# Kernel tuning notes

Measured on AMD Instinct MI355X. Metric: run time of the kernel, lower is better.

The kernel has to match this reference:

```python
import jax, jax.numpy as jnp
import numpy as np

B, L = 16, 1024
D_MODEL = 384
EXPAND = 2
D_INNER = EXPAND * D_MODEL  # 768
D_STATE = 16
D_CONV = 4
DT_RANK = (D_MODEL + 15) // 16  # 24


def _causal_conv(x, w, b):
    # x: (B,L,Di); w: (Di,K) depthwise kernel; b: (Di,). Causal: pad K-1 on the left.
    K = w.shape[1]
    Lx = x.shape[1]
    xp = jnp.pad(x, ((0, 0), (K - 1, 0), (0, 0)))
    out = sum(xp[:, k:k + Lx, :] * w[:, k] for k in range(K)) + b
    return out


def _selective_scan(u, delta, A, Bm, Cm, Dv):
    # u, delta: (B,L,Di); A: (Di,N); Bm, Cm: (B,L,N); Dv: (Di,)
    def step(h, inp):
        dt, bt, ct, ut = inp  # (B,Di),(B,N),(B,N),(B,Di)
        dA = jnp.exp(dt[..., None] * A)                     # (B,Di,N)
        h = h * dA + (dt * ut)[..., None] * bt[:, None, :]  # (B,Di,N)
        y = jnp.einsum('bdn,bn->bd', h, ct)
        return h, y

    h0 = jnp.zeros((u.shape[0], u.shape[2], A.shape[1]), u.dtype)
    xs = (delta.swapaxes(0, 1), Bm.swapaxes(0, 1), Cm.swapaxes(0, 1), u.swapaxes(0, 1))
    _, ys = jax.lax.scan(step, h0, xs)
    return ys.swapaxes(0, 1) + u * Dv


def _mamba_dir(xz, conv_w, conv_bias, xproj_w, dt_w, dt_b, A_log, Dv):
    xh, z = jnp.split(xz, 2, axis=-1)                 # each (B,L,Di)
    xh = jax.nn.silu(_causal_conv(xh, conv_w, conv_bias))
    dbc = xh @ xproj_w.T                              # (B,L,DT_RANK+2N)
    dt, Bm, Cm = jnp.split(dbc, [DT_RANK, DT_RANK + D_STATE], axis=-1)
    delta = jax.nn.softplus(dt @ dt_w.T + dt_b)       # (B,L,Di)
    A = -jnp.exp(A_log)                               # (Di,N)
    y = _selective_scan(xh, delta, A, Bm, Cm, Dv)
    return y * jax.nn.silu(z)


def setup_inputs():
    key = jax.random.key(0)
    ks = jax.random.split(key, 16)

    def rn(k, shape, s):
        return jax.random.normal(k, shape, dtype=jnp.float32) * s

    A_init = jnp.log(jnp.tile(jnp.arange(1, D_STATE + 1, dtype=jnp.float32), (D_INNER, 1)))
    return dict(
        x=rn(ks[0], (B, L, D_MODEL), 1.0),
        ln_w=jnp.ones((D_MODEL,), jnp.float32),
        ln_b=jnp.zeros((D_MODEL,), jnp.float32),
        in_proj_w=rn(ks[1], (2 * D_INNER, D_MODEL), 0.02),
        out_proj_w=rn(ks[2], (D_MODEL, D_INNER), 0.02),
        conv_w_fwd=rn(ks[3], (D_INNER, D_CONV), 0.2),
        conv_bias_fwd=jnp.zeros((D_INNER,), jnp.float32),
        xproj_w_fwd=rn(ks[4], (DT_RANK + 2 * D_STATE, D_INNER), 0.02),
        dt_w_fwd=rn(ks[5], (D_INNER, DT_RANK), 0.1),
        dt_b_fwd=jnp.full((D_INNER,), -4.0, jnp.float32),
        A_log_fwd=A_init,
        D_fwd=jnp.ones((D_INNER,), jnp.float32),
        conv_w_bwd=rn(ks[6], (D_INNER, D_CONV), 0.2),
        conv_bias_bwd=jnp.zeros((D_INNER,), jnp.float32),
        xproj_w_bwd=rn(ks[7], (DT_RANK + 2 * D_STATE, D_INNER), 0.02),
        dt_w_bwd=rn(ks[8], (D_INNER, DT_RANK), 0.1),
        dt_b_bwd=jnp.full((D_INNER,), -4.0, jnp.float32),
        A_log_bwd=A_init,
        D_bwd=jnp.ones((D_INNER,), jnp.float32),
    )


def reference(x, ln_w, ln_b, in_proj_w, out_proj_w,
              conv_w_fwd, conv_bias_fwd, xproj_w_fwd, dt_w_fwd, dt_b_fwd, A_log_fwd, D_fwd,
              conv_w_bwd, conv_bias_bwd, xproj_w_bwd, dt_w_bwd, dt_b_bwd, A_log_bwd, D_bwd):
    # LayerNorm
    mu = x.mean(-1, keepdims=True)
    var = ((x - mu) ** 2).mean(-1, keepdims=True)
    xn = (x - mu) / jnp.sqrt(var + 1e-5) * ln_w + ln_b
    # Shared input projection -> (B,L,2*Di)
    xz = xn @ in_proj_w.T
    # Forward-direction mamba branch
    out_f = _mamba_dir(xz, conv_w_fwd, conv_bias_fwd, xproj_w_fwd, dt_w_fwd, dt_b_fwd, A_log_fwd, D_fwd)
    # Backward-direction branch on sequence-flipped xz, flipped back (bimamba v2)
    out_r = _mamba_dir(xz[:, ::-1], conv_w_bwd, conv_bias_bwd, xproj_w_bwd, dt_w_bwd, dt_b_bwd, A_log_bwd, D_bwd)[:, ::-1]
    # Output projection + residual (drop_path=0 -> identity)
    return x + (out_f + out_r) @ out_proj_w.T
```

## Files before the change

kernel.cpp:

```cpp
#include <hip/hip_runtime.h>
#include <cstdint>
#include <cstddef>

#define BN_   16
#define LN_   1024
#define DM_   384
#define DI_   768
#define NS_   16
#define RDT_  24
#define NDBC_ 56
#define NDBCP 64
#define NC_   16
#define LC_   64

typedef unsigned short ushortT;
typedef short bf16x8 __attribute__((ext_vector_type(8)));
typedef float f32x4 __attribute__((ext_vector_type(4)));

typedef __attribute__((address_space(3))) uint32_t lds_u32_t;
typedef __attribute__((address_space(1))) const uint32_t glb_u32_t;

static __device__ __forceinline__ void stage16(const void* g, void* lds) {
    __builtin_amdgcn_global_load_lds(
        (glb_u32_t*)(uintptr_t)g,
        (lds_u32_t*)(uint32_t)(uintptr_t)lds,
        16, 0, 0);
}

static __device__ __forceinline__ float silu_f(float x) {
    return x / (1.0f + __expf(-x));
}
static __device__ __forceinline__ float softplus_f(float s) {
    return fmaxf(s, 0.0f) + __logf(1.0f + __expf(-fabsf(s)));
}
static __device__ __forceinline__ ushortT f2bf(float f) {
    union { float f; uint32_t u; } v; v.f = f;
    uint32_t u = v.u;
    uint32_t r = u + 0x7fffu + ((u >> 16) & 1u);
    return (ushortT)(r >> 16);
}
static __device__ __forceinline__ float bf2f(ushortT b) {
    union { uint32_t u; float f; } v; v.u = ((uint32_t)b) << 16;
    return v.f;
}

__global__ __launch_bounds__(256) void wconv_kernel(
    const float* __restrict__ w1, int n1, const float* __restrict__ w2, int n2,
    const float* __restrict__ xwf, const float* __restrict__ xwb,
    ushortT* __restrict__ o1, ushortT* __restrict__ o2,
    ushortT* __restrict__ oxf, ushortT* __restrict__ oxb)
{
    int i = blockIdx.x * 256 + threadIdx.x;
    if (i < n1) { o1[i] = f2bf(w1[i]); return; }
    i -= n1;
    if (i < n2) { o2[i] = f2bf(w2[i]); return; }
    i -= n2;
    const int nx = NDBCP * DI_;
    if (i < 2 * nx) {
        int which = i >= nx;
        int j = which ? (i - nx) : i;
        int row = j / DI_;
        const float* src = which ? xwb : xwf;
        ushortT* dst = which ? oxb : oxf;
        dst[j] = (row < NDBC_) ? f2bf(src[j]) : (ushortT)0;
    }
}

__global__ __launch_bounds__(256) void ln_kernel(
    const float* __restrict__ x, const float* __restrict__ w,
    const float* __restrict__ b, ushortT* __restrict__ xn,
    int row0, int nrows)
{
    int r = blockIdx.x * 4 + (threadIdx.x >> 6);
    if (r >= nrows) return;
    int lane = threadIdx.x & 63;
    const float* xr = x + (size_t)(row0 + r) * DM_;
    float v[6];
    float s = 0.0f;
#pragma unroll
    for (int i = 0; i < 6; i++) { v[i] = xr[lane + 64 * i]; s += v[i]; }
#pragma unroll
    for (int o = 32; o > 0; o >>= 1) s += __shfl_down(s, o, 64);
    s = __shfl(s, 0, 64);
    float mu = s * (1.0f / DM_);
    float q = 0.0f;
#pragma unroll
    for (int i = 0; i < 6; i++) { float d = v[i] - mu; q += d * d; }
#pragma unroll
    for (int o = 32; o > 0; o >>= 1) q += __shfl_down(q, o, 64);
    q = __shfl(q, 0, 64);
    float rstd = rsqrtf(q * (1.0f / DM_) + 1e-5f);
    ushortT* outp = xn + (size_t)r * DM_;
#pragma unroll
    for (int i = 0; i < 6; i++) {
        int c = lane + 64 * i;
        outp[c] = f2bf((v[i] - mu) * rstd * w[c] + b[c]);
    }
}

template <int BM, int BN, int WR, int WC, bool CAT, bool RES, bool OB>
__global__ __launch_bounds__(256) void gemm_mfma(
    const ushortT* __restrict__ Aa, const ushortT* __restrict__ Ab_,
    const ushortT* __restrict__ W, const float* __restrict__ R,
    void* __restrict__ Cv, int M, int N, int Khalf)
{
    constexpr int WTM = BM / WR;
    constexpr int WTN = BN / WC;
    constexpr int FM = WTM / 16;
    constexpr int FN = WTN / 16;
    __shared__ ushortT As[BM * 32];
    __shared__ ushortT Ws[BN * 32];
    int tid = threadIdx.x;
    int bm = blockIdx.x * BM, bn = blockIdx.y * BN;
    int wave = tid >> 6, lane = tid & 63;
    int wm = wave % WR, wn = wave / WR;
    f32x4 acc[FM][FN] = {};
    int Ktot = CAT ? 2 * Khalf : Khalf;
    int lrow = lane >> 2;
    int lk = (lane & 3) * 8;

    for (int k0 = 0; k0 < Ktot; k0 += 32) {
        const ushortT* Asrc = (!CAT || k0 < Khalf) ? Aa : Ab_;
        int ka = (!CAT || k0 < Khalf) ? k0 : (k0 - Khalf);
        __syncthreads();
#pragma unroll
        for (int c = 0; c < BM / 64; c++) {
            int ch = c * 4 + wave;
            int row = ch * 16 + lrow;
            stage16(Asrc + (size_t)(bm + row) * Khalf + ka + lk, &As[ch * 16 * 32]);
        }
#pragma unroll
        for (int c = 0; c < BN / 64; c++) {
            int ch = c * 4 + wave;
            int row = ch * 16 + lrow;
            stage16(W + (size_t)(bn + row) * Khalf + ka + lk, &Ws[ch * 16 * 32]);
        }
        __syncthreads();
        int mb = (wm * WTM + (lane & 15)) * 32 + (lane >> 4) * 8;
        int nb = (wn * WTN + (lane & 15)) * 32 + (lane >> 4) * 8;
        bf16x8 af[FM], bfr[FN];
#pragma unroll
        for (int mi = 0; mi < FM; mi++) af[mi] = *(bf16x8*)&As[mb + mi * 16 * 32];
#pragma unroll
        for (int ni = 0; ni < FN; ni++) bfr[ni] = *(bf16x8*)&Ws[nb + ni * 16 * 32];
#pragma unroll
        for (int mi = 0; mi < FM; mi++)
#pragma unroll
            for (int ni = 0; ni < FN; ni++)
                acc[mi][ni] = __builtin_amdgcn_mfma_f32_16x16x32_bf16(
                    af[mi], bfr[ni], acc[mi][ni], 0, 0, 0);
    }

#pragma unroll
    for (int mi = 0; mi < FM; mi++) {
        int row = bm + wm * WTM + 16 * mi + (lane >> 4) * 4;
#pragma unroll
        for (int ni = 0; ni < FN; ni++) {
            int col = bn + wn * WTN + 16 * ni + (lane & 15);
#pragma unroll
            for (int r = 0; r < 4; r++) {
                size_t o = (size_t)(row + r) * N + col;
                float v = acc[mi][ni][r];
                if (RES) v += R[o];
                if (OB) ((ushortT*)Cv)[o] = f2bf(v);
                else    ((float*)Cv)[o] = v;
            }
        }
    }
}

__global__ __launch_bounds__(256) void conv_kernel(
    const ushortT* __restrict__ XZ,
    const float* __restrict__ wf, const float* __restrict__ bf,
    const float* __restrict__ wb, const float* __restrict__ bb,
    ushortT* __restrict__ XH, int gB)
{
    const int D8 = DI_ / 8;
    int idx = blockIdx.x * 256 + threadIdx.x;
    int perdir = gB * LN_ * D8;
    int dir = 0;
    if (idx >= perdir) { idx -= perdir; dir = 1; }
    int d8 = idx % D8;
    int l = (idx / D8) & (LN_ - 1);
    int b = idx / (D8 * LN_);
    int d = d8 * 8;
    const float* cw = (dir ? wb : wf) + d * 4;
    const float* cb = (dir ? bb : bf) + d;

    float xv[4][8];
#pragma unroll
    for (int k = 0; k < 4; k++) {
        int j = l - 3 + k;
        if (j < 0) {
#pragma unroll
            for (int c = 0; c < 8; c++) xv[k][c] = 0.0f;
        } else {
            int ls = dir ? (LN_ - 1 - j) : j;
            ushort4 v = *(const ushort4*)(XZ + (size_t)(b * LN_ + ls) * (2 * DI_) + d);
            ushort4 v2 = *(const ushort4*)(XZ + (size_t)(b * LN_ + ls) * (2 * DI_) + d + 4);
            xv[k][0] = bf2f(v.x);  xv[k][1] = bf2f(v.y);
            xv[k][2] = bf2f(v.z);  xv[k][3] = bf2f(v.w);
            xv[k][4] = bf2f(v2.x); xv[k][5] = bf2f(v2.y);
            xv[k][6] = bf2f(v2.z); xv[k][7] = bf2f(v2.w);
        }
    }
    ushortT out[8];
#pragma unroll
    for (int c = 0; c < 8; c++) {
        float4 w4 = *(const float4*)(cw + c * 4);
        float s = cb[c];
        s = fmaf(xv[0][c], w4.x, s);
        s = fmaf(xv[1][c], w4.y, s);
        s = fmaf(xv[2][c], w4.z, s);
        s = fmaf(xv[3][c], w4.w, s);
        out[c] = f2bf(silu_f(s));
    }
    ushortT* op = XH + ((size_t)dir * gB * LN_ + (size_t)(b * LN_ + l)) * DI_ + d;
    *(ushort4*)(op + 0) = make_ushort4(out[0], out[1], out[2], out[3]);
    *(ushort4*)(op + 4) = make_ushort4(out[4], out[5], out[6], out[7]);
}

__global__ __launch_bounds__(256) void xproj_mfma(
    const ushortT* __restrict__ XH, const ushortT* __restrict__ Wf,
    const ushortT* __restrict__ Wb, float* __restrict__ Cf,
    float* __restrict__ Cb, int mblocksPerDir)
{
    __shared__ ushortT As[64 * 32];
    __shared__ ushortT Ws[64 * 32];
    int blk = blockIdx.x;
    int dir = blk >= mblocksPerDir;
    const ushortT* W = dir ? Wb : Wf;
    float* C = dir ? Cb : Cf;
    int bmG = blk * 64;
    int bmC = (blk - dir * mblocksPerDir) * 64;
    int tid = threadIdx.x, wave = tid >> 6, lane = tid & 63;
    f32x4 acc[4] = {};
    int lrow = lane >> 2;
    int lk = (lane & 3) * 8;

    for (int k0 = 0; k0 < DI_; k0 += 32) {
        __syncthreads();
        stage16(XH + (size_t)(bmG + wave * 16 + lrow) * DI_ + k0 + lk, &As[wave * 16 * 32]);
        stage16(W + (size_t)(wave * 16 + lrow) * DI_ + k0 + lk, &Ws[wave * 16 * 32]);
        __syncthreads();
        bf16x8 bfr = *(bf16x8*)&Ws[(wave * 16 + (lane & 15)) * 32 + (lane >> 4) * 8];
#pragma unroll
        for (int mi = 0; mi < 4; mi++) {
            bf16x8 af = *(bf16x8*)&As[(mi * 16 + (lane & 15)) * 32 + (lane >> 4) * 8];
            acc[mi] = __builtin_amdgcn_mfma_f32_16x16x32_bf16(af, bfr, acc[mi], 0, 0, 0);
        }
    }
#pragma unroll
    for (int mi = 0; mi < 4; mi++) {
        int row = bmC + 16 * mi + (lane >> 4) * 4;
        int col = wave * 16 + (lane & 15);
#pragma unroll
        for (int r = 0; r < 4; r++)
            C[(size_t)(row + r) * NDBCP + col] = acc[mi][r];
    }
}

__global__ __launch_bounds__(256) void scan1_kernel(
    const ushortT* __restrict__ XH,
    const float* __restrict__ dbcf, const float* __restrict__ dbcb,
    const float* __restrict__ dtwf, const float* __restrict__ dtbf,
    const float* __restrict__ alogf,
    const float* __restrict__ dtwb, const float* __restrict__ dtbb,
    const float* __restrict__ alogb,
    uint32_t* __restrict__ UD,
    float* __restrict__ hs1, float* __restrict__ dec, int gB)
{
    int bid = blockIdx.x;
    int c = bid % NC_; bid /= NC_;
    int dchunk = bid % 3; bid /= 3;
    int b = bid % gB;
    int dir = bid / gB;
    int d = dchunk * 256 + threadIdx.x;

    const ushortT* xh = XH + (size_t)dir * gB * LN_ * DI_;
    const float* dbc  = dir ? dbcb : dbcf;
    const float* dtw  = (dir ? dtwb : dtwf) + d * RDT_;
    float dtb         = (dir ? dtbb : dtbf)[d];
    const float* alog = dir ? alogb : alogf;

    float An[NS_];
#pragma unroll
    for (int n = 0; n < NS_; n++) An[n] = -__expf(alog[d * NS_ + n]);
    float a1 = An[0];
    bool pk = true;
#pragma unroll
    for (int n = 0; n < NS_; n++)
        pk = pk && (fabsf(An[n] - (float)(n + 1) * a1) <=
                    1e-3f * (float)(n + 1) * fabsf(a1) + 1e-6f);
    pk = (bool)__all((int)pk);

    float wrow[RDT_];
#pragma unroll
    for (int r = 0; r < RDT_; r++) wrow[r] = dtw[r];

    __shared__ float sdbc[LC_ * NDBCP];
    int rb = b * LN_ + c * LC_;
    int jb = c * LC_;
#pragma unroll
    for (int i = 0; i < 4; i++) {
        int idx = threadIdx.x + 256 * i;
        int row = idx >> 4, c4 = (idx & 15) * 4;
        *(float4*)&sdbc[row * NDBCP + c4] =
            *(const float4*)(dbc + (size_t)(rb + row) * NDBCP + c4);
    }
    __syncthreads();

    float h[NS_];
#pragma unroll
    for (int n = 0; n < NS_; n++) h[n] = 0.0f;
    float S = 0.0f;
    uint32_t* udp = UD + (size_t)((dir * gB + b) * LN_ + jb) * DI_ + d;

    if (pk) {
        for (int lr = 0; lr < LC_; lr++) {
            const float4* rp4 = (const float4*)&sdbc[lr * NDBCP];
            float4 t0 = rp4[0], t1 = rp4[1], t2 = rp4[2];
            float4 t3 = rp4[3], t4 = rp4[4], t5 = rp4[5];
            float s0 = dtb, s1 = 0.f, s2 = 0.f, s3 = 0.f;
            s0 = fmaf(t0.x, wrow[0], s0);  s1 = fmaf(t0.y, wrow[1], s1);
            s2 = fmaf(t0.z, wrow[2], s2);  s3 = fmaf(t0.w, wrow[3], s3);
            s0 = fmaf(t1.x, wrow[4], s0);  s1 = fmaf(t1.y, wrow[5], s1);
            s2 = fmaf(t1.z, wrow[6], s2);  s3 = fmaf(t1.w, wrow[7], s3);
            s0 = fmaf(t2.x, wrow[8], s0);  s1 = fmaf(t2.y, wrow[9], s1);
            s2 = fmaf(t2.z, wrow[10], s2); s3 = fmaf(t2.w, wrow[11], s3);
            s0 = fmaf(t3.x, wrow[12], s0); s1 = fmaf(t3.y, wrow[13], s1);
            s2 = fmaf(t3.z, wrow[14], s2); s3 = fmaf(t3.w, wrow[15], s3);
            s0 = fmaf(t4.x, wrow[16], s0); s1 = fmaf(t4.y, wrow[17], s1);
            s2 = fmaf(t4.z, wrow[18], s2); s3 = fmaf(t4.w, wrow[19], s3);
            s0 = fmaf(t5.x, wrow[20], s0); s1 = fmaf(t5.y, wrow[21], s1);
            s2 = fmaf(t5.z, wrow[22], s2); s3 = fmaf(t5.w, wrow[23], s3);
            float dt = softplus_f((s0 + s1) + (s2 + s3));
            S += dt;
            float u = bf2f(xh[(rb + lr) * DI_ + d]);
            udp[lr * DI_] = ((uint32_t)f2bf(dt) << 16) | (uint32_t)f2bf(u);
            float du = dt * u;
            float4 B0 = rp4[6], B1 = rp4[7], B2 = rp4[8], B3 = rp4[9];
            const float* Bp = (const float*)&B0;
            float Bv[NS_] = {B0.x, B0.y, B0.z, B0.w, B1.x, B1.y, B1.z, B1.w,
                             B2.x, B2.y, B2.z, B2.w, B3.x, B3.y, B3.z, B3.w};
            (void)Bp;
            float q1 = __expf(dt * a1);
            float q2 = q1 * q1, q4 = q2 * q2, q8 = q4 * q4;
            float p2 = q2, p3 = q2 * q1, p5 = q4 * q1, p6 = q4 * q2, p7 = q4 * p3;
            float pw[NS_] = {q1, p2, p3, q4, p5, p6, p7, q8,
                             q8 * q1, q8 * p2, q8 * p3, q8 * q4,
                             q8 * p5, q8 * p6, q8 * p7, q8 * q8};
#pragma unroll
            for (int n = 0; n < NS_; n++)
                h[n] = fmaf(h[n], pw[n], du * Bv[n]);
        }
        float q1 = __expf(S * a1);
        float q2 = q1 * q1, q4 = q2 * q2, q8 = q4 * q4;
        float p2 = q2, p3 = q2 * q1, p5 = q4 * q1, p6 = q4 * q2, p7 = q4 * p3;
        float pw[NS_] = {q1, p2, p3, q4, p5, p6, p7, q8,
                         q8 * q1, q8 * p2, q8 * p3, q8 * q4,
                         q8 * p5, q8 * p6, q8 * p7, q8 * q8};
        int si = (((dir * gB + b) * NC_ + c) * DI_ + d) * NS_;
#pragma unroll
        for (int n = 0; n < NS_; n++) {
            hs1[si + n] = h[n];
            dec[si + n] = pw[n];
        }
    } else {
        for (int lr = 0; lr < LC_; lr++) {
            const float* rowp = &sdbc[lr * NDBCP];
            float s0 = dtb, s1 = 0.f, s2 = 0.f, s3 = 0.f;
#pragma unroll
            for (int r = 0; r < 6; r++) {
                s0 = fmaf(rowp[r], wrow[r], s0);
                s1 = fmaf(rowp[6 + r], wrow[6 + r], s1);
                s2 = fmaf(rowp[12 + r], wrow[12 + r], s2);
                s3 = fmaf(rowp[18 + r], wrow[18 + r], s3);
            }
            float dt = softplus_f((s0 + s1) + (s2 + s3));
            S += dt;
            float u = bf2f(xh[(rb + lr) * DI_ + d]);
            udp[lr * DI_] = ((uint32_t)f2bf(dt) << 16) | (uint32_t)f2bf(u);
            float du = dt * u;
#pragma unroll
            for (int n = 0; n < NS_; n++)
                h[n] = fmaf(h[n], __expf(dt * An[n]), du * rowp[RDT_ + n]);
        }
        int si = (((dir * gB + b) * NC_ + c) * DI_ + d) * NS_;
#pragma unroll
        for (int n = 0; n < NS_; n++) {
            hs1[si + n] = h[n];
            dec[si + n] = __expf(An[n] * S);
        }
    }
}

__global__ __launch_bounds__(256) void scan2_kernel(
    const float* __restrict__ hs1, const float* __restrict__ dec,
    float* __restrict__ hin, int gB)
{
    int e = blockIdx.x * 256 + threadIdx.x;
    int n = e & 15; int e2 = e >> 4;
    int d = e2 % DI_; e2 /= DI_;
    int b = e2 % gB; int dir = e2 / gB;
    int base = (((dir * gB + b) * NC_) * DI_ + d) * NS_ + n;
    float h = 0.0f;
    const int cs = DI_ * NS_;
    for (int c = 0; c < NC_; c++) {
        int idx = base + c * cs;
        hin[idx] = h;
        h = fmaf(h, dec[idx], hs1[idx]);
    }
}

__global__ __launch_bounds__(256) void scan3_kernel(
    const uint32_t* __restrict__ UD, const ushortT* __restrict__ XZ,
    const float* __restrict__ dbcf, const float* __restrict__ dbcb,
    const float* __restrict__ alogf, const float* __restrict__ dvf,
    const float* __restrict__ alogb, const float* __restrict__ dvb,
    const float* __restrict__ hin,
    ushortT* __restrict__ yf, ushortT* __restrict__ yb, int gB)
{
    int bid = blockIdx.x;
    int c = bid % NC_; bid /= NC_;
    int dchunk = bid % 3; bid /= 3;
    int b = bid % gB;
    int dir = bid / gB;
    int d = dchunk * 256 + threadIdx.x;

    const float* dbc  = dir ? dbcb : dbcf;
    const float* alog = dir ? alogb : alogf;
    float Dd          = (dir ? dvb : dvf)[d];
    ushortT* y        = dir ? yb : yf;

    float An[NS_];
#pragma unroll
    for (int n = 0; n < NS_; n++) An[n] = -__expf(alog[d * NS_ + n]);
    float a1 = An[0];
    bool pk = true;
#pragma unroll
    for (int n = 0; n < NS_; n++)
        pk = pk && (fabsf(An[n] - (float)(n + 1) * a1) <=
                    1e-3f * (float)(n + 1) * fabsf(a1) + 1e-6f);
    pk = (bool)__all((int)pk);

    __shared__ float sBC[LC_ * 32];
    int rb = b * LN_ + c * LC_;
    int jb = c * LC_;
#pragma unroll
    for (int i = 0; i < 2; i++) {
        int idx = threadIdx.x + 256 * i;
        int row = idx >> 3, c4 = (idx & 7) * 4;
        *(float4*)&sBC[row * 32 + c4] =
            *(const float4*)(dbc + (size_t)(rb + row) * NDBCP + RDT_ + c4);
    }
    __syncthreads();

    int si = (((dir * gB + b) * NC_ + c) * DI_ + d) * NS_;
    float h[NS_];
#pragma unroll
    for (int n = 0; n < NS_; n++) h[n] = hin[si + n];
    const uint32_t* udp = UD + (size_t)((dir * gB + b) * LN_ + jb) * DI_ + d;

    if (pk) {
        for (int lr = 0; lr < LC_; lr++) {
            const float4* rp4 = (const float4*)&sBC[lr * 32];
            float4 B0 = rp4[0], B1 = rp4[1], B2 = rp4[2], B3 = rp4[3];
            float4 C0 = rp4[4], C1 = rp4[5], C2 = rp4[6], C3 = rp4[7];
            float Bv[NS_] = {B0.x, B0.y, B0.z, B0.w, B1.x, B1.y, B1.z, B1.w,
                             B2.x, B2.y, B2.z, B2.w, B3.x, B3.y, B3.z, B3.w};
            float Cw[NS_] = {C0.x, C0.y, C0.z, C0.w, C1.x, C1.y, C1.z, C1.w,
                             C2.x, C2.y, C2.z, C2.w, C3.x, C3.y, C3.z, C3.w};
            uint32_t ud = udp[lr * DI_];
            float u = bf2f((ushortT)(ud & 0xffffu));
            float dt = bf2f((ushortT)(ud >> 16));
            float du = dt * u;
            float q1 = __expf(dt * a1);
            float q2 = q1 * q1, q4 = q2 * q2, q8 = q4 * q4;
            float p2 = q2, p3 = q2 * q1, p5 = q4 * q1, p6 = q4 * q2, p7 = q4 * p3;
            float pw[NS_] = {q1, p2, p3, q4, p5, p6, p7, q8,
                             q8 * q1, q8 * p2, q8 * p3, q8 * q4,
                             q8 * p5, q8 * p6, q8 * p7, q8 * q8};
            float y0 = 0.f, y1 = 0.f, y2 = 0.f, y3 = 0.f;
#pragma unroll
            for (int n = 0; n < NS_; n += 4) {
                h[n + 0] = fmaf(h[n + 0], pw[n + 0], du * Bv[n + 0]);
                h[n + 1] = fmaf(h[n + 1], pw[n + 1], du * Bv[n + 1]);
                h[n + 2] = fmaf(h[n + 2], pw[n + 2], du * Bv[n + 2]);
                h[n + 3] = fmaf(h[n + 3], pw[n + 3], du * Bv[n + 3]);
                y0 = fmaf(h[n + 0], Cw[n + 0], y0);
                y1 = fmaf(h[n + 1], Cw[n + 1], y1);
                y2 = fmaf(h[n + 2], Cw[n + 2], y2);
                y3 = fmaf(h[n + 3], Cw[n + 3], y3);
            }
            float yv = ((y0 + y1) + (y2 + y3)) + u * Dd;
            int j = jb + lr;
            int lo = dir ? (LN_ - 1 - j) : j;
            float z = bf2f(XZ[(size_t)(b * LN_ + lo) * (2 * DI_) + DI_ + d]);
            y[(b * LN_ + lo) * DI_ + d] = f2bf(yv * silu_f(z));
        }
    } else {
        for (int lr = 0; lr < LC_; lr++) {
            const float* rowp = &sBC[lr * 32];
            uint32_t ud = udp[lr * DI_];
            float u = bf2f((ushortT)(ud & 0xffffu));
            float dt = bf2f((ushortT)(ud >> 16));
            float du = dt * u;
            float y0 = 0.f, y1 = 0.f, y2 = 0.f, y3 = 0.f;
#pragma unroll
            for (int n = 0; n < NS_; n += 4) {
                h[n + 0] = fmaf(h[n + 0], __expf(dt * An[n + 0]), du * rowp[n + 0]);
                h[n + 1] = fmaf(h[n + 1], __expf(dt * An[n + 1]), du * rowp[n + 1]);
                h[n + 2] = fmaf(h[n + 2], __expf(dt * An[n + 2]), du * rowp[n + 2]);
                h[n + 3] = fmaf(h[n + 3], __expf(dt * An[n + 3]), du * rowp[n + 3]);
                y0 = fmaf(h[n + 0], rowp[16 + n + 0], y0);
                y1 = fmaf(h[n + 1], rowp[16 + n + 1], y1);
                y2 = fmaf(h[n + 2], rowp[16 + n + 2], y2);
                y3 = fmaf(h[n + 3], rowp[16 + n + 3], y3);
            }
            float yv = ((y0 + y1) + (y2 + y3)) + u * Dd;
            int j = jb + lr;
            int lo = dir ? (LN_ - 1 - j) : j;
            float z = bf2f(XZ[(size_t)(b * LN_ + lo) * (2 * DI_) + DI_ + d]);
            y[(b * LN_ + lo) * DI_ + d] = f2bf(yv * silu_f(z));
        }
    }
}

extern "C" void kernel_launch(void* const* d_in, const int* in_sizes, int n_in,
                              void* d_out, int out_size, void* d_ws, size_t ws_size,
                              hipStream_t stream)
{
    const float* x         = (const float*)d_in[0];
    const float* ln_w      = (const float*)d_in[1];
    const float* ln_b      = (const float*)d_in[2];
    const float* in_proj_w = (const float*)d_in[3];
    const float* out_proj_w= (const float*)d_in[4];
    const float* conv_wf   = (const float*)d_in[5];
    const float* conv_bf   = (const float*)d_in[6];
    const float* xproj_f   = (const float*)d_in[7];
    const float* dt_wf     = (const float*)d_in[8];
    const float* dt_bf     = (const float*)d_in[9];
    const float* alog_f    = (const float*)d_in[10];
    const float* dv_f      = (const float*)d_in[11];
    const float* conv_wb   = (const float*)d_in[12];
    const float* conv_bb   = (const float*)d_in[13];
    const float* xproj_b   = (const float*)d_in[14];
    const float* dt_wb     = (const float*)d_in[15];
    const float* dt_bb     = (const float*)d_in[16];
    const float* alog_b    = (const float*)d_in[17];
    const float* dv_b      = (const float*)d_in[18];
    float* outp = (float*)d_out;

    const int n_w1 = 2 * DI_ * DM_;
    const int n_w2 = DM_ * DI_;
    const int n_wx = NDBCP * DI_;

    uint8_t* base = (uint8_t*)d_ws;
    size_t off = 0;
    auto alloc = [&](size_t nbytes) {
        uint8_t* r = base + off;
        off = (off + nbytes + 255) & ~(size_t)255;
        return r;
    };
    ushortT* WbIn  = (ushortT*)alloc((size_t)n_w1 * 2);
    ushortT* WbOut = (ushortT*)alloc((size_t)n_w2 * 2);
    ushortT* WbXf  = (ushortT*)alloc((size_t)n_wx * 2);
    ushortT* WbXb  = (ushortT*)alloc((size_t)n_wx * 2);
    size_t fixed_bytes = off;

    size_t per_b_bytes = 23ull * 1024 * 1024;
    int g = BN_;
    while (g > 1 && fixed_bytes + (size_t)g * per_b_bytes + (1ull << 20) > ws_size) g >>= 1;

    wconv_kernel<<<(n_w1 + n_w2 + 2 * n_wx + 255) / 256, 256, 0, stream>>>(
        in_proj_w, n_w1, out_proj_w, n_w2, xproj_f, xproj_b,
        WbIn, WbOut, WbXf, WbXb);

    for (int b0 = 0; b0 < BN_; b0 += g) {
        int rows = g * LN_;
        off = fixed_bytes;
        ushortT* XNb = (ushortT*)alloc((size_t)rows * DM_ * 2);
        ushortT* XZ  = (ushortT*)alloc((size_t)rows * 2 * DI_ * 2);
        ushortT* XH  = (ushortT*)alloc((size_t)2 * rows * DI_ * 2);
        float* DBCf  = (float*)alloc((size_t)rows * NDBCP * 4);
        float* DBCb  = (float*)alloc((size_t)rows * NDBCP * 4);
        uint32_t* UD = (uint32_t*)alloc((size_t)2 * rows * DI_ * 4);
        size_t st_n  = (size_t)2 * g * NC_ * DI_ * NS_;
        float* HS1   = (float*)alloc(st_n * 4);
        float* DEC   = (float*)alloc(st_n * 4);
        float* HIN   = (float*)alloc(st_n * 4);
        ushortT* Yf  = (ushortT*)alloc((size_t)rows * DI_ * 2);
        ushortT* Yb  = (ushortT*)alloc((size_t)rows * DI_ * 2);
        int row0 = b0 * LN_;

        ln_kernel<<<rows / 4, 256, 0, stream>>>(x, ln_w, ln_b, XNb, row0, rows);

        gemm_mfma<128, 128, 2, 2, false, false, true>
            <<<dim3(rows / 128, (2 * DI_) / 128), 256, 0, stream>>>(
            XNb, nullptr, WbIn, nullptr, XZ, rows, 2 * DI_, DM_);

        conv_kernel<<<(2 * rows * (DI_ / 8)) / 256, 256, 0, stream>>>(
            XZ, conv_wf, conv_bf, conv_wb, conv_bb, XH, g);

        xproj_mfma<<<2 * (rows / 64), 256, 0, stream>>>(
            XH, WbXf, WbXb, DBCf, DBCb, rows / 64);

        scan1_kernel<<<2 * g * 3 * NC_, 256, 0, stream>>>(
            XH, DBCf, DBCb, dt_wf, dt_bf, alog_f,
            dt_wb, dt_bb, alog_b, UD, HS1, DEC, g);

        scan2_kernel<<<(2 * g * DI_ * NS_) / 256, 256, 0, stream>>>(HS1, DEC, HIN, g);

        scan3_kernel<<<2 * g * 3 * NC_, 256, 0, stream>>>(
            UD, XZ, DBCf, DBCb, alog_f, dv_f, alog_b, dv_b,
            HIN, Yf, Yb, g);

        gemm_mfma<64, 128, 1, 4, true, true, false>
            <<<dim3(rows / 64, DM_ / 128), 256, 0, stream>>>(
            Yf, Yb, WbOut, x + (size_t)row0 * DM_,
            outp + (size_t)row0 * DM_, rows, DM_, DI_);
    }
}
```

Baseline: 506.2 us.

## Move dt projection out of scan into a separate MFMA kernel producing UD

The dt low-rank projection (24-wide dot per element), the softplus and the packing of dt and u into UD move out of scan1 into a new dtud_kernel that uses bf16 MFMA. xproj now also writes the dt slice as padded bf16, and dt_w is converted to bf16. scan1 then only reads the packed UD and B, with 8-step batched loads, and scan3 also prefetches UD and z in batches of 8. This takes FMA work and serial latency off the scan's critical path, at the cost of an extra kernel launch, extra UD traffic and lower precision for the dt computation.

```diff
diff --git a/kernel.cpp b/kernel.cpp
--- a/kernel.cpp
+++ b/kernel.cpp
@@ -47,8 +47,10 @@
 __global__ __launch_bounds__(256) void wconv_kernel(
     const float* __restrict__ w1, int n1, const float* __restrict__ w2, int n2,
     const float* __restrict__ xwf, const float* __restrict__ xwb,
+    const float* __restrict__ dwf, const float* __restrict__ dwb,
     ushortT* __restrict__ o1, ushortT* __restrict__ o2,
-    ushortT* __restrict__ oxf, ushortT* __restrict__ oxb)
+    ushortT* __restrict__ oxf, ushortT* __restrict__ oxb,
+    ushortT* __restrict__ odf, ushortT* __restrict__ odb)
 {
     int i = blockIdx.x * 256 + threadIdx.x;
     if (i < n1) { o1[i] = f2bf(w1[i]); return; }
@@ -63,6 +65,17 @@
         const float* src = which ? xwb : xwf;
         ushortT* dst = which ? oxb : oxf;
         dst[j] = (row < NDBC_) ? f2bf(src[j]) : (ushortT)0;
+        return;
+    }
+    i -= 2 * nx;
+    const int nd = DI_ * 32;
+    if (i < 2 * nd) {
+        int which = i >= nd;
+        int j = which ? (i - nd) : i;
+        int row = j >> 5, col = j & 31;
+        const float* src = which ? dwb : dwf;
+        ushortT* dst = which ? odb : odf;
+        dst[j] = (col < RDT_) ? f2bf(src[row * RDT_ + col]) : (ushortT)0;
     }
 }
 
@@ -223,7 +236,7 @@
 __global__ __launch_bounds__(256) void xproj_mfma(
     const ushortT* __restrict__ XH, const ushortT* __restrict__ Wf,
     const ushortT* __restrict__ Wb, float* __restrict__ Cf,
-    float* __restrict__ Cb, int mblocksPerDir)
+    float* __restrict__ Cb, ushortT* __restrict__ DT24, int mblocksPerDir)
 {
     __shared__ ushortT As[64 * 32];
     __shared__ ushortT Ws[64 * 32];
@@ -258,16 +271,80 @@
         for (int r = 0; r < 4; r++)
             C[(size_t)(row + r) * NDBCP + col] = acc[mi][r];
     }
+    if (wave < 2) {
+        ushortT* dtp = DT24 + (size_t)dir * (size_t)(mblocksPerDir * 64) * 32;
+        int col = wave * 16 + (lane & 15);
+#pragma unroll
+        for (int mi = 0; mi < 4; mi++) {
+            int row = bmC + 16 * mi + (lane >> 4) * 4;
+#pragma unroll
+            for (int r = 0; r < 4; r++)
+                dtp[(size_t)(row + r) * 32 + col] =
+                    (col < RDT_) ? f2bf(acc[mi][r]) : (ushortT)0;
+        }
+    }
+}
+
+__global__ __launch_bounds__(256) void dtud_kernel(
+    const ushortT* __restrict__ DT24, const ushortT* __restrict__ WDtf,
+    const ushortT* __restrict__ WDtb,
+    const float* __restrict__ dtbf, const float* __restrict__ dtbb,
+    const ushortT* __restrict__ XH, uint32_t* __restrict__ UD, int rows)
+{
+    __shared__ ushortT As[128 * 32];
+    __shared__ ushortT Ws[64 * 32];
+    int dir = blockIdx.z;
+    int bm = blockIdx.x * 128;
+    int bn = blockIdx.y * 64;
+    const ushortT* A = DT24 + (size_t)dir * rows * 32;
+    const ushortT* W = dir ? WDtb : WDtf;
+    const float* dtb = dir ? dtbb : dtbf;
+    const ushortT* xh = XH + (size_t)dir * rows * DI_;
+    uint32_t* ud = UD + (size_t)dir * rows * DI_;
+    int tid = threadIdx.x, wave = tid >> 6, lane = tid & 63;
+    int lrow = lane >> 2, lk = (lane & 3) * 8;
+
+    stage16(A + (size_t)(bm + wave * 16 + lrow) * 32 + lk, &As[wave * 16 * 32]);
+    stage16(A + (size_t)(bm + 64 + wave * 16 + lrow) * 32 + lk, &As[(64 + wave * 16) * 32]);
+    stage16(W + (size_t)(bn + wave * 16 + lrow) * 32 + lk, &Ws[wave * 16 * 32]);
+    __syncthreads();
+
+    f32x4 acc[2][4] = {};
+    bf16x8 bfr[4];
+#pragma unroll
+    for (int ni = 0; ni < 4; ni++)
+        bfr[ni] = *(bf16x8*)&Ws[(ni * 16 + (lane & 15)) * 32 + (lane >> 4) * 8];
+#pragma unroll
+    for (int mi = 0; mi < 2; mi++) {
+        bf16x8 af = *(bf16x8*)&As[(wave * 32 + mi * 16 + (lane & 15)) * 32 + (lane >> 4) * 8];
+#pragma unroll
+        for (int ni = 0; ni < 4; ni++)
+            acc[mi][ni] = __builtin_amdgcn_mfma_f32_16x16x32_bf16(
+                af, bfr[ni], acc[mi][ni], 0, 0, 0);
+    }
+#pragma unroll
+    for (int ni = 0; ni < 4; ni++) {
+        int d = bn + ni * 16 + (lane & 15);
+        float bias = dtb[d];
+#pragma unroll
+        for (int mi = 0; mi < 2; mi++) {
+            int rb = bm + wave * 32 + mi * 16 + (lane >> 4) * 4;
+#pragma unroll
+            for (int r = 0; r < 4; r++) {
+                int row = rb + r;
+                float dt = softplus_f(acc[mi][ni][r] + bias);
+                float u = bf2f(xh[(size_t)row * DI_ + d]);
+                ud[(size_t)row * DI_ + d] =
+                    ((uint32_t)f2bf(dt) << 16) | (uint32_t)f2bf(u);
+            }
+        }
+    }
 }
 
 __global__ __launch_bounds__(256) void scan1_kernel(
-    const ushortT* __restrict__ XH,
+    const uint32_t* __restrict__ UD,
     const float* __restrict__ dbcf, const float* __restrict__ dbcb,
-    const float* __restrict__ dtwf, const float* __restrict__ dtbf,
-    const float* __restrict__ alogf,
-    const float* __restrict__ dtwb, const float* __restrict__ dtbb,
-    const float* __restrict__ alogb,
-    uint32_t* __restrict__ UD,
+    const float* __restrict__ alogf, const float* __restrict__ alogb,
     float* __restrict__ hs1, float* __restrict__ dec, int gB)
 {
     int bid = blockIdx.x;
@@ -277,10 +354,7 @@
     int dir = bid / gB;
     int d = dchunk * 256 + threadIdx.x;
 
-    const ushortT* xh = XH + (size_t)dir * gB * LN_ * DI_;
     const float* dbc  = dir ? dbcb : dbcf;
-    const float* dtw  = (dir ? dtwb : dtwf) + d * RDT_;
-    float dtb         = (dir ? dtbb : dtbf)[d];
     const float* alog = dir ? alogb : alogf;
 
     float An[NS_];
@@ -294,19 +368,13 @@
                     1e-3f * (float)(n + 1) * fabsf(a1) + 1e-6f);
     pk = (bool)__all((int)pk);
 
-    float wrow[RDT_];
-#pragma unroll
-    for (int r = 0; r < RDT_; r++) wrow[r] = dtw[r];
-
-    __shared__ float sdbc[LC_ * NDBCP];
+    __shared__ float sB[LC_ * 16];
     int rb = b * LN_ + c * LC_;
     int jb = c * LC_;
-#pragma unroll
-    for (int i = 0; i < 4; i++) {
-        int idx = threadIdx.x + 256 * i;
-        int row = idx >> 4, c4 = (idx & 15) * 4;
-        *(float4*)&sdbc[row * NDBCP + c4] =
-            *(const float4*)(dbc + (size_t)(rb + row) * NDBCP + c4);
+    {
+        int row = threadIdx.x >> 2, c4 = (threadIdx.x & 3) * 4;
+        *(float4*)&sB[row * 16 + c4] =
+            *(const float4*)(dbc + (size_t)(rb + row) * NDBCP + RDT_ + c4);
     }
     __syncthreads();
 
@@ -314,45 +382,34 @@
 #pragma unroll
     for (int n = 0; n < NS_; n++) h[n] = 0.0f;
     float S = 0.0f;
-    uint32_t* udp = UD + (size_t)((dir * gB + b) * LN_ + jb) * DI_ + d;
+    const uint32_t* udp = UD + (size_t)((dir * gB + b) * LN_ + jb) * DI_ + d;
 
     if (pk) {
-        for (int lr = 0; lr < LC_; lr++) {
-            const float4* rp4 = (const float4*)&sdbc[lr * NDBCP];
-            float4 t0 = rp4[0], t1 = rp4[1], t2 = rp4[2];
-            float4 t3 = rp4[3], t4 = rp4[4], t5 = rp4[5];
-            float s0 = dtb, s1 = 0.f, s2 = 0.f, s3 = 0.f;
-            s0 = fmaf(t0.x, wrow[0], s0);  s1 = fmaf(t0.y, wrow[1], s1);
-            s2 = fmaf(t0.z, wrow[2], s2);  s3 = fmaf(t0.w, wrow[3], s3);
-            s0 = fmaf(t1.x, wrow[4], s0);  s1 = fmaf(t1.y, wrow[5], s1);
-            s2 = fmaf(t1.z, wrow[6], s2);  s3 = fmaf(t1.w, wrow[7], s3);
-            s0 = fmaf(t2.x, wrow[8], s0);  s1 = fmaf(t2.y, wrow[9], s1);
-            s2 = fmaf(t2.z, wrow[10], s2); s3 = fmaf(t2.w, wrow[11], s3);
-            s0 = fmaf(t3.x, wrow[12], s0); s1 = fmaf(t3.y, wrow[13], s1);
-            s2 = fmaf(t3.z, wrow[14], s2); s3 = fmaf(t3.w, wrow[15], s3);
-            s0 = fmaf(t4.x, wrow[16], s0); s1 = fmaf(t4.y, wrow[17], s1);
-            s2 = fmaf(t4.z, wrow[18], s2); s3 = fmaf(t4.w, wrow[19], s3);
-            s0 = fmaf(t5.x, wrow[20], s0); s1 = fmaf(t5.y, wrow[21], s1);
-            s2 = fmaf(t5.z, wrow[22], s2); s3 = fmaf(t5.w, wrow[23], s3);
-            float dt = softplus_f((s0 + s1) + (s2 + s3));
-            S += dt;
-            float u = bf2f(xh[(rb + lr) * DI_ + d]);
-            udp[lr * DI_] = ((uint32_t)f2bf(dt) << 16) | (uint32_t)f2bf(u);
-            float du = dt * u;
-            float4 B0 = rp4[6], B1 = rp4[7], B2 = rp4[8], B3 = rp4[9];
-            const float* Bp = (const float*)&B0;
-            float Bv[NS_] = {B0.x, B0.y, B0.z, B0.w, B1.x, B1.y, B1.z, B1.w,
-                             B2.x, B2.y, B2.z, B2.w, B3.x, B3.y, B3.z, B3.w};
-            (void)Bp;
-            float q1 = __expf(dt * a1);
-            float q2 = q1 * q1, q4 = q2 * q2, q8 = q4 * q4;
-            float p2 = q2, p3 = q2 * q1, p5 = q4 * q1, p6 = q4 * q2, p7 = q4 * p3;
-            float pw[NS_] = {q1, p2, p3, q4, p5, p6, p7, q8,
-                             q8 * q1, q8 * p2, q8 * p3, q8 * q4,
-                             q8 * p5, q8 * p6, q8 * p7, q8 * q8};
-#pragma unroll
-            for (int n = 0; n < NS_; n++)
-                h[n] = fmaf(h[n], pw[n], du * Bv[n]);
+        for (int lt = 0; lt < LC_; lt += 8) {
+            uint32_t ud8[8];
+#pragma unroll
+            for (int i = 0; i < 8; i++) ud8[i] = udp[(lt + i) * DI_];
+#pragma unroll
+            for (int i = 0; i < 8; i++) {
+                int lr = lt + i;
+                const float4* Bp4 = (const float4*)&sB[lr * 16];
+                float4 B0 = Bp4[0], B1 = Bp4[1], B2 = Bp4[2], B3 = Bp4[3];
+                float Bv[NS_] = {B0.x, B0.y, B0.z, B0.w, B1.x, B1.y, B1.z, B1.w,
+                                 B2.x, B2.y, B2.z, B2.w, B3.x, B3.y, B3.z, B3.w};
+                float u = bf2f((ushortT)(ud8[i] & 0xffffu));
+                float dt = bf2f((ushortT)(ud8[i] >> 16));
+                S += dt;
+                float du = dt * u;
+                float q1 = __expf(dt * a1);
+                float q2 = q1 * q1, q4 = q2 * q2, q8 = q4 * q4;
+                float p2 = q2, p3 = q2 * q1, p5 = q4 * q1, p6 = q4 * q2, p7 = q4 * p3;
+                float pw[NS_] = {q1, p2, p3, q4, p5, p6, p7, q8,
+                                 q8 * q1, q8 * p2, q8 * p3, q8 * q4,
+                                 q8 * p5, q8 * p6, q8 * p7, q8 * q8};
+#pragma unroll
+                for (int n = 0; n < NS_; n++)
+                    h[n] = fmaf(h[n], pw[n], du * Bv[n]);
+            }
         }
         float q1 = __expf(S * a1);
         float q2 = q1 * q1, q4 = q2 * q2, q8 = q4 * q4;
@@ -368,23 +425,15 @@
         }
     } else {
         for (int lr = 0; lr < LC_; lr++) {
-            const float* rowp = &sdbc[lr * NDBCP];
-            float s0 = dtb, s1 = 0.f, s2 = 0.f, s3 = 0.f;
-#pragma unroll
-            for (int r = 0; r < 6; r++) {
-                s0 = fmaf(rowp[r], wrow[r], s0);
-                s1 = fmaf(rowp[6 + r], wrow[6 + r], s1);
-                s2 = fmaf(rowp[12 + r], wrow[12 + r], s2);
-                s3 = fmaf(rowp[18 + r], wrow[18 + r], s3);
-            }
-            float dt = softplus_f((s0 + s1) + (s2 + s3));
+            const float* rowp = &sB[lr * 16];
+            uint32_t udv = udp[lr * DI_];
+            float u = bf2f((ushortT)(udv & 0xffffu));
+            float dt = bf2f((ushortT)(udv >> 16));
             S += dt;
-            float u = bf2f(xh[(rb + lr) * DI_ + d]);
-            udp[lr * DI_] = ((uint32_t)f2bf(dt) << 16) | (uint32_t)f2bf(u);
             float du = dt * u;
 #pragma unroll
             for (int n = 0; n < NS_; n++)
-                h[n] = fmaf(h[n], __expf(dt * An[n]), du * rowp[RDT_ + n]);
+                h[n] = fmaf(h[n], __expf(dt * An[n]), du * rowp[n]);
         }
         int si = (((dir * gB + b) * NC_ + c) * DI_ + d) * NS_;
 #pragma unroll
@@ -463,41 +512,53 @@
     const uint32_t* udp = UD + (size_t)((dir * gB + b) * LN_ + jb) * DI_ + d;
 
     if (pk) {
-        for (int lr = 0; lr < LC_; lr++) {
-            const float4* rp4 = (const float4*)&sBC[lr * 32];
-            float4 B0 = rp4[0], B1 = rp4[1], B2 = rp4[2], B3 = rp4[3];
-            float4 C0 = rp4[4], C1 = rp4[5], C2 = rp4[6], C3 = rp4[7];
-            float Bv[NS_] = {B0.x, B0.y, B0.z, B0.w, B1.x, B1.y, B1.z, B1.w,
-                             B2.x, B2.y, B2.z, B2.w, B3.x, B3.y, B3.z, B3.w};
-            float Cw[NS_] = {C0.x, C0.y, C0.z, C0.w, C1.x, C1.y, C1.z, C1.w,
-                             C2.x, C2.y, C2.z, C2.w, C3.x, C3.y, C3.z, C3.w};
-            uint32_t ud = udp[lr * DI_];
-            float u = bf2f((ushortT)(ud & 0xffffu));
-            float dt = bf2f((ushortT)(ud >> 16));
-            float du = dt * u;
-            float q1 = __expf(dt * a1);
-            float q2 = q1 * q1, q4 = q2 * q2, q8 = q4 * q4;
-            float p2 = q2, p3 = q2 * q1, p5 = q4 * q1, p6 = q4 * q2, p7 = q4 * p3;
-            float pw[NS_] = {q1, p2, p3, q4, p5, p6, p7, q8,
-                             q8 * q1, q8 * p2, q8 * p3, q8 * q4,
-                             q8 * p5, q8 * p6, q8 * p7, q8 * q8};
-            float y0 = 0.f, y1 = 0.f, y2 = 0.f, y3 = 0.f;
-#pragma unroll
-            for (int n = 0; n < NS_; n += 4) {
-                h[n + 0] = fmaf(h[n + 0], pw[n + 0], du * Bv[n + 0]);
-                h[n + 1] = fmaf(h[n + 1], pw[n + 1], du * Bv[n + 1]);
-                h[n + 2] = fmaf(h[n + 2], pw[n + 2], du * Bv[n + 2]);
-                h[n + 3] = fmaf(h[n + 3], pw[n + 3], du * Bv[n + 3]);
-                y0 = fmaf(h[n + 0], Cw[n + 0], y0);
-                y1 = fmaf(h[n + 1], Cw[n + 1], y1);
-                y2 = fmaf(h[n + 2], Cw[n + 2], y2);
-                y3 = fmaf(h[n + 3], Cw[n + 3], y3);
+        for (int lt = 0; lt < LC_; lt += 8) {
+            uint32_t ud8[8];
+            ushortT z8[8];
+#pragma unroll
+            for (int i = 0; i < 8; i++) {
+                ud8[i] = udp[(lt + i) * DI_];
+                int j = jb + lt + i;
+                int lo = dir ? (LN_ - 1 - j) : j;
+                z8[i] = XZ[(size_t)(b * LN_ + lo) * (2 * DI_) + DI_ + d];
             }
-            float yv = ((y0 + y1) + (y2 + y3)) + u * Dd;
-            int j = jb + lr;
-            int lo = dir ? (LN_ - 1 - j) : j;
-            float z = bf2f(XZ[(size_t)(b * LN_ + lo) * (2 * DI_) + DI_ + d]);
-            y[(b * LN_ + lo) * DI_ + d] = f2bf(yv * silu_f(z));
+#pragma unroll
+            for (int i = 0; i < 8; i++) {
+                int lr = lt + i;
+                const float4* rp4 = (const float4*)&sBC[lr * 32];
+                float4 B0 = rp4[0], B1 = rp4[1], B2 = rp4[2], B3 = rp4[3];
+                float4 C0 = rp4[4], C1 = rp4[5], C2 = rp4[6], C3 = rp4[7];
+                float Bv[NS_] = {B0.x, B0.y, B0.z, B0.w, B1.x, B1.y, B1.z, B1.w,
+                                 B2.x, B2.y, B2.z, B2.w, B3.x, B3.y, B3.z, B3.w};
+                float Cw[NS_] = {C0.x, C0.y, C0.z, C0.w, C1.x, C1.y, C1.z, C1.w,
+                                 C2.x, C2.y, C2.z, C2.w, C3.x, C3.y, C3.z, C3.w};
+                float u = bf2f((ushortT)(ud8[i] & 0xffffu));
+                float dt = bf2f((ushortT)(ud8[i] >> 16));
+                float du = dt * u;
+                float q1 = __expf(dt * a1);
+                float q2 = q1 * q1, q4 = q2 * q2, q8 = q4 * q4;
+                float p2 = q2, p3 = q2 * q1, p5 = q4 * q1, p6 = q4 * q2, p7 = q4 * p3;
+                float pw[NS_] = {q1, p2, p3, q4, p5, p6, p7, q8,
+                                 q8 * q1, q8 * p2, q8 * p3, q8 * q4,
+                                 q8 * p5, q8 * p6, q8 * p7, q8 * q8};
+                float y0 = 0.f, y1 = 0.f, y2 = 0.f, y3 = 0.f;
+#pragma unroll
+                for (int n = 0; n < NS_; n += 4) {
+                    h[n + 0] = fmaf(h[n + 0], pw[n + 0], du * Bv[n + 0]);
+                    h[n + 1] = fmaf(h[n + 1], pw[n + 1], du * Bv[n + 1]);
+                    h[n + 2] = fmaf(h[n + 2], pw[n + 2], du * Bv[n + 2]);
+                    h[n + 3] = fmaf(h[n + 3], pw[n + 3], du * Bv[n + 3]);
+                    y0 = fmaf(h[n + 0], Cw[n + 0], y0);
+                    y1 = fmaf(h[n + 1], Cw[n + 1], y1);
+                    y2 = fmaf(h[n + 2], Cw[n + 2], y2);
+                    y3 = fmaf(h[n + 3], Cw[n + 3], y3);
+                }
+                float yv = ((y0 + y1) + (y2 + y3)) + u * Dd;
+                int j = jb + lr;
+                int lo = dir ? (LN_ - 1 - j) : j;
+                float z = bf2f(z8[i]);
+                y[(b * LN_ + lo) * DI_ + d] = f2bf(yv * silu_f(z));
+            }
         }
     } else {
         for (int lr = 0; lr < LC_; lr++) {
@@ -555,6 +616,7 @@
     const int n_w1 = 2 * DI_ * DM_;
     const int n_w2 = DM_ * DI_;
     const int n_wx = NDBCP * DI_;
+    const int n_wd = DI_ * 32;
 
     uint8_t* base = (uint8_t*)d_ws;
     size_t off = 0;
@@ -567,31 +629,34 @@
     ushortT* WbOut = (ushortT*)alloc((size_t)n_w2 * 2);
     ushortT* WbXf  = (ushortT*)alloc((size_t)n_wx * 2);
     ushortT* WbXb  = (ushortT*)alloc((size_t)n_wx * 2);
+    ushortT* WbDtf = (ushortT*)alloc((size_t)n_wd * 2);
+    ushortT* WbDtb = (ushortT*)alloc((size_t)n_wd * 2);
     size_t fixed_bytes = off;
 
-    size_t per_b_bytes = 23ull * 1024 * 1024;
+    size_t per_b_bytes = 24ull * 1024 * 1024;
     int g = BN_;
     while (g > 1 && fixed_bytes + (size_t)g * per_b_bytes + (1ull << 20) > ws_size) g >>= 1;
 
-    wconv_kernel<<<(n_w1 + n_w2 + 2 * n_wx + 255) / 256, 256, 0, stream>>>(
-        in_proj_w, n_w1, out_proj_w, n_w2, xproj_f, xproj_b,
-        WbIn, WbOut, WbXf, WbXb);
+    wconv_kernel<<<(n_w1 + n_w2 + 2 * n_wx + 2 * n_wd + 255) / 256, 256, 0, stream>>>(
+        in_proj_w, n_w1, out_proj_w, n_w2, xproj_f, xproj_b, dt_wf, dt_wb,
+        WbIn, WbOut, WbXf, WbXb, WbDtf, WbDtb);
 
     for (int b0 = 0; b0 < BN_; b0 += g) {
         int rows = g * LN_;
         off = fixed_bytes;
-        ushortT* XNb = (ushortT*)alloc((size_t)rows * DM_ * 2);
-        ushortT* XZ  = (ushortT*)alloc((size_t)rows * 2 * DI_ * 2);
-        ushortT* XH  = (ushortT*)alloc((size_t)2 * rows * DI_ * 2);
-        float* DBCf  = (float*)alloc((size_t)rows * NDBCP * 4);
-        float* DBCb  = (float*)alloc((size_t)rows * NDBCP * 4);
-        uint32_t* UD = (uint32_t*)alloc((size_t)2 * rows * DI_ * 4);
-        size_t st_n  = (size_t)2 * g * NC_ * DI_ * NS_;
-        float* HS1   = (float*)alloc(st_n * 4);
-        float* DEC   = (float*)alloc(st_n * 4);
-        float* HIN   = (float*)alloc(st_n * 4);
-        ushortT* Yf  = (ushortT*)alloc((size_t)rows * DI_ * 2);
-        ushortT* Yb  = (ushortT*)alloc((size_t)rows * DI_ * 2);
+        ushortT* XNb  = (ushortT*)alloc((size_t)rows * DM_ * 2);
+        ushortT* XZ   = (ushortT*)alloc((size_t)rows * 2 * DI_ * 2);
+        ushortT* XH   = (ushortT*)alloc((size_t)2 * rows * DI_ * 2);
+        float* DBCf   = (float*)alloc((size_t)rows * NDBCP * 4);
+        float* DBCb   = (float*)alloc((size_t)rows * NDBCP * 4);
+        ushortT* DT24 = (ushortT*)alloc((size_t)2 * rows * 32 * 2);
+        uint32_t* UD  = (uint32_t*)alloc((size_t)2 * rows * DI_ * 4);
+        size_t st_n   = (size_t)2 * g * NC_ * DI_ * NS_;
+        float* HS1    = (float*)alloc(st_n * 4);
+        float* DEC    = (float*)alloc(st_n * 4);
+        float* HIN    = (float*)alloc(st_n * 4);
+        ushortT* Yf   = (ushortT*)alloc((size_t)rows * DI_ * 2);
+        ushortT* Yb   = (ushortT*)alloc((size_t)rows * DI_ * 2);
         int row0 = b0 * LN_;
 
         ln_kernel<<<rows / 4, 256, 0, stream>>>(x, ln_w, ln_b, XNb, row0, rows);
@@ -604,11 +669,13 @@
             XZ, conv_wf, conv_bf, conv_wb, conv_bb, XH, g);
 
         xproj_mfma<<<2 * (rows / 64), 256, 0, stream>>>(
-            XH, WbXf, WbXb, DBCf, DBCb, rows / 64);
+            XH, WbXf, WbXb, DBCf, DBCb, DT24, rows / 64);
+
+        dtud_kernel<<<dim3(rows / 128, DI_ / 64, 2), 256, 0, stream>>>(
+            DT24, WbDtf, WbDtb, dt_bf, dt_bb, XH, UD, rows);
 
         scan1_kernel<<<2 * g * 3 * NC_, 256, 0, stream>>>(
-            XH, DBCf, DBCb, dt_wf, dt_bf, alog_f,
-            dt_wb, dt_bb, alog_b, UD, HS1, DEC, g);
+            UD, DBCf, DBCb, alog_f, alog_b, HS1, DEC, g);
 
         scan2_kernel<<<(2 * g * DI_ * NS_) / 256, 256, 0, stream>>>(HS1, DEC, HIN, g);
 
```

Result: no change. 511.8 us (+1.1%).
